# Kernel tuning notes

Hardware: AMD Instinct MI355X
Metric: run time of the kernel (lower is better)

The kernel has to match this reference:

```python
import jax, jax.numpy as jnp
import numpy as np

NUM_HEADS = 12
HEAD_DIM = 64  # d_out // num_heads = 768 // 12


def setup_inputs() -> dict:
    key = jax.random.key(0)
    k1, k2 = jax.random.split(key)
    x = jax.random.normal(k1, (2, 2048, 768), dtype=jnp.float32)
    # torch Linear weight: [d_out, d_in], y = x @ W.T
    Wq = jax.random.normal(k2, (768, 768), dtype=jnp.float32) * 0.02
    return {"x": x, "Wq": Wq}


def reference(x, Wq):
    b, n, d_in = x.shape
    H, hd = NUM_HEADS, HEAD_DIM
    d_out = H * hd
    # NOTE: the original module uses Wq for queries, keys AND values.
    qkv = x @ Wq.T                                   # [b, n, d_out]
    h = qkv.reshape(b, n, H, hd).transpose(0, 2, 1, 3)  # [b, H, n, hd]
    scores = jnp.einsum('bhqd,bhkd->bhqk', h, h)      # [b, H, n, n]
    causal = jnp.triu(jnp.ones((n, n), dtype=bool), k=1)
    scores = jnp.where(causal, -jnp.inf, scores)
    attn = jax.nn.softmax(scores / jnp.sqrt(jnp.float32(hd)), axis=-1)
    ctx = jnp.einsum('bhqk,bhkd->bhqd', attn, h)      # [b, H, n, hd]
    # faithful to source: transpose(-2,-1) -> [b, H, hd, n], then view(b, n, d_out)
    ctx = ctx.transpose(0, 1, 3, 2)
    return ctx.reshape(b, n, d_out)
```

## Files before the change

kernel.cpp:

```cpp
#include <hip/hip_runtime.h>
#include <math.h>

typedef __attribute__((ext_vector_type(8))) short  short8;
typedef __attribute__((ext_vector_type(4))) float  floatx4;

#define MFMA16(a, b, c) __builtin_amdgcn_mfma_f32_16x16x32_bf16(a, b, c, 0, 0, 0)

constexpr int NSEQ = 2048;
constexpr int DIN  = 768;
constexpr int NH   = 12;
constexpr float QSCALE = 0.18033688011112042f;

constexpr int PK = 72;

__device__ __forceinline__ ushort f2bf(float f) {
    unsigned u = __float_as_uint(f);
    u += 0x7FFF + ((u >> 16) & 1);
    return (ushort)(u >> 16);
}
__device__ __forceinline__ float bf2f(ushort u) {
    return __uint_as_float(((unsigned)u) << 16);
}
__device__ __forceinline__ unsigned cvt_pk_bf16(float lo, float hi) {
    unsigned r;
    asm("v_cvt_pk_bf16_f32 %0, %1, %2" : "=v"(r) : "v"(lo), "v"(hi));
    return r;
}
__device__ __forceinline__ short8 pk8(float4 a, float4 b) {
    union { unsigned u[4]; short8 s; } r;
    r.u[0] = cvt_pk_bf16(a.x, a.y);
    r.u[1] = cvt_pk_bf16(a.z, a.w);
    r.u[2] = cvt_pk_bf16(b.x, b.y);
    r.u[3] = cvt_pk_bf16(b.z, b.w);
    return r.s;
}
__device__ __forceinline__ void bar_lds() {
    asm volatile("s_waitcnt lgkmcnt(0)" ::: "memory");
    __builtin_amdgcn_s_barrier();
}

__global__ __launch_bounds__(256, 3)
void qkv_mfma(const float* __restrict__ x, const float* __restrict__ Wq,
              ushort* __restrict__ h)
{
    __shared__ ushort As[2][64 * PK];
    __shared__ ushort Bs[2][64 * PK];

    const int tid  = threadIdx.x;
    const int w    = tid >> 6;
    const int lane = tid & 63;
    const int m    = lane & 15;
    const int quad = lane >> 4;
    const int r0   = blockIdx.x * 64;
    const int c0   = blockIdx.y * 64;
    const int mrow0 = (w & 1) * 32;
    const int ncol0 = (w >> 1) * 32;

    const int srow = tid >> 3;
    const int scol = (tid & 7) * 8;

    floatx4 C[2][2] = {};
    float4 arf[2][2], brf[2][2];

    #pragma unroll
    for (int i = 0; i < 2; ++i) {
        const float* ax = x  + (size_t)(r0 + srow + i * 32) * DIN + scol;
        const float* bx = Wq + (size_t)(c0 + srow + i * 32) * DIN + scol;
        arf[i][0] = ((const float4*)ax)[0]; arf[i][1] = ((const float4*)ax)[1];
        brf[i][0] = ((const float4*)bx)[0]; brf[i][1] = ((const float4*)bx)[1];
    }
    #pragma unroll
    for (int i = 0; i < 2; ++i) {
        *(short8*)&As[0][(srow + i * 32) * PK + scol] = pk8(arf[i][0], arf[i][1]);
        *(short8*)&Bs[0][(srow + i * 32) * PK + scol] = pk8(brf[i][0], brf[i][1]);
    }
    #pragma unroll
    for (int i = 0; i < 2; ++i) {
        const float* ax = x  + (size_t)(r0 + srow + i * 32) * DIN + 64 + scol;
        const float* bx = Wq + (size_t)(c0 + srow + i * 32) * DIN + 64 + scol;
        arf[i][0] = ((const float4*)ax)[0]; arf[i][1] = ((const float4*)ax)[1];
        brf[i][0] = ((const float4*)bx)[0]; brf[i][1] = ((const float4*)bx)[1];
    }
    bar_lds();

    for (int kk = 0; kk < 12; ++kk) {
        const int cur = kk & 1;

        #pragma unroll
        for (int kt2 = 0; kt2 < 2; ++kt2) {
            short8 a0 = *(const short8*)&As[cur][(mrow0 + m)      * PK + kt2 * 32 + quad * 8];
            short8 a1 = *(const short8*)&As[cur][(mrow0 + 16 + m) * PK + kt2 * 32 + quad * 8];
            short8 b0 = *(const short8*)&Bs[cur][(ncol0 + m)      * PK + kt2 * 32 + quad * 8];
            short8 b1 = *(const short8*)&Bs[cur][(ncol0 + 16 + m) * PK + kt2 * 32 + quad * 8];
            C[0][0] = MFMA16(a0, b0, C[0][0]);
            C[0][1] = MFMA16(a0, b1, C[0][1]);
            C[1][0] = MFMA16(a1, b0, C[1][0]);
            C[1][1] = MFMA16(a1, b1, C[1][1]);
        }

        if (kk + 1 < 12) {
            const int nxt = cur ^ 1;
            #pragma unroll
            for (int i = 0; i < 2; ++i) {
                *(short8*)&As[nxt][(srow + i * 32) * PK + scol] = pk8(arf[i][0], arf[i][1]);
                *(short8*)&Bs[nxt][(srow + i * 32) * PK + scol] = pk8(brf[i][0], brf[i][1]);
            }
            if (kk + 2 < 12) {
                const int k0 = (kk + 2) * 64;
                #pragma unroll
                for (int i = 0; i < 2; ++i) {
                    const float* ax = x  + (size_t)(r0 + srow + i * 32) * DIN + k0 + scol;
                    const float* bx = Wq + (size_t)(c0 + srow + i * 32) * DIN + k0 + scol;
                    arf[i][0] = ((const float4*)ax)[0]; arf[i][1] = ((const float4*)ax)[1];
                    brf[i][0] = ((const float4*)bx)[0]; brf[i][1] = ((const float4*)bx)[1];
                }
            }
            bar_lds();
        }
    }

    #pragma unroll
    for (int mt = 0; mt < 2; ++mt)
        #pragma unroll
        for (int nt = 0; nt < 2; ++nt) {
            int cg = c0 + ncol0 + nt * 16 + m;
            int head = cg >> 6, d = cg & 63;
            #pragma unroll
            for (int r = 0; r < 4; ++r) {
                int rg = r0 + mrow0 + mt * 16 + quad * 4 + r;
                int b = rg >> 11, q = rg & 2047;
                h[((size_t)(b * NH + head) * NSEQ + q) * 64 + d] = f2bf(C[mt][nt][r]);
            }
        }
}

__global__ __launch_bounds__(256, 6)
void attn_mfma(const ushort* __restrict__ h, float* __restrict__ out)
{
    __shared__ ushort Ks[64 * PK];
    __shared__ ushort Vt[64 * PK];
    __shared__ ushort Ps[2 * 16 * PK];

    const int tid  = threadIdx.x;
    const int w    = tid >> 6;
    const int lane = tid & 63;
    const int m    = lane & 15;
    const int quad = lane >> 4;
    const int qsub = w & 1;
    const int khalf= w >> 1;

    const int xi = blockIdx.x;
    const int bh = blockIdx.y;
    const int qt = ((bh >> 2) & 1) ? xi : (63 - xi);
    const int q0 = qt * 32;
    const int wq = q0 + qsub * 16;
    const int nkt = (qt >> 1) + 1;
    const ushort* __restrict__ Hh = h + (size_t)bh * NSEQ * 64;
    ushort* Psw = Ps + qsub * 16 * PK;

    const int kr2  = (tid & 31) * 2;
    const int part = tid >> 5;
    const int db   = part * 8;

    short8 qa[2];
    #pragma unroll
    for (int kt2 = 0; kt2 < 2; ++kt2) {
        short8 raw = *(const short8*)(Hh + (size_t)(wq + m) * 64 + kt2 * 32 + quad * 8);
        #pragma unroll
        for (int j = 0; j < 8; ++j)
            qa[kt2][j] = (short)f2bf(bf2f((ushort)raw[j]) * QSCALE);
    }

    floatx4 O[4] = {};
    float lacc = 0.0f;

    short8 pre0, pre1;
    {
        const ushort* src = Hh + (size_t)kr2 * 64 + db;
        pre0 = *(const short8*)src;
        pre1 = *(const short8*)(src + 64);
    }

    for (int kt = 0; kt < nkt; ++kt) {
        bar_lds();

        *(short8*)&Ks[kr2       * PK + db] = pre0;
        *(short8*)&Ks[(kr2 + 1) * PK + db] = pre1;
        union { short8 v; ushort u[8]; } ua, ub;
        ua.v = pre0; ub.v = pre1;
        #pragma unroll
        for (int i = 0; i < 8; ++i)
            *(unsigned*)&Vt[(db + i) * PK + kr2] =
                (unsigned)ua.u[i] | ((unsigned)ub.u[i] << 16);
        if (kt + 1 < nkt) {
            const ushort* src = Hh + (size_t)((kt + 1) * 64 + kr2) * 64 + db;
            pre0 = *(const short8*)src;
            pre1 = *(const short8*)(src + 64);
        }
        bar_lds();

        floatx4 S[2] = {};
        #pragma unroll
        for (int kt2 = 0; kt2 < 2; ++kt2)
            #pragma unroll
            for (int mt2 = 0; mt2 < 2; ++mt2) {
                short8 ka = *(const short8*)
                    &Ks[(khalf * 32 + mt2 * 16 + m) * PK + kt2 * 32 + quad * 8];
                S[mt2] = MFMA16(ka, qa[kt2], S[mt2]);
            }

        const int lim  = wq + m - kt * 64;
        const bool diag = (kt == nkt - 1);
        #pragma unroll
        for (int mt2 = 0; mt2 < 2; ++mt2) {
            const int kb = (khalf * 2 + mt2) * 16 + quad * 4;
            float p0, p1, p2, p3;
            if (diag) {
                p0 = (kb + 0 <= lim) ? exp2f(S[mt2][0]) : 0.0f;
                p1 = (kb + 1 <= lim) ? exp2f(S[mt2][1]) : 0.0f;
                p2 = (kb + 2 <= lim) ? exp2f(S[mt2][2]) : 0.0f;
                p3 = (kb + 3 <= lim) ? exp2f(S[mt2][3]) : 0.0f;
            } else {
                p0 = exp2f(S[mt2][0]);
                p1 = exp2f(S[mt2][1]);
                p2 = exp2f(S[mt2][2]);
                p3 = exp2f(S[mt2][3]);
            }
            lacc += (p0 + p1) + (p2 + p3);
            uint2 pw;
            pw.x = cvt_pk_bf16(p0, p1);
            pw.y = cvt_pk_bf16(p2, p3);
            *(uint2*)&Psw[m * PK + kb] = pw;
        }

        short8 pb = *(const short8*)&Psw[m * PK + khalf * 32 + quad * 8];
        #pragma unroll
        for (int mt = 0; mt < 4; ++mt) {
            short8 va = *(const short8*)
                &Vt[(mt * 16 + m) * PK + khalf * 32 + quad * 8];
            O[mt] = MFMA16(va, pb, O[mt]);
        }
    }

    lacc += __shfl_xor(lacc, 16);
    lacc += __shfl_xor(lacc, 32);

    float* Om = (float*)&Ks[0];
    float* Lm = Om + 2 * 64 * 17;
    bar_lds();
    if (khalf == 1) {
        #pragma unroll
        for (int mt = 0; mt < 4; ++mt)
            #pragma unroll
            for (int r = 0; r < 4; ++r) {
                int d = mt * 16 + quad * 4 + r;
                Om[(qsub * 64 + d) * 17 + m] = O[mt][r];
            }
        if (quad == 0) Lm[qsub * 16 + m] = lacc;
    }
    bar_lds();
    if (khalf == 0) {
        float linv = 1.0f / (lacc + Lm[qsub * 16 + m]);
        #pragma unroll
        for (int mt = 0; mt < 4; ++mt)
            #pragma unroll
            for (int r = 0; r < 4; ++r) {
                int d = mt * 16 + quad * 4 + r;
                float v = O[mt][r] + Om[(qsub * 64 + d) * 17 + m];
                out[((size_t)bh * 64 + d) * NSEQ + q0 + qsub * 16 + m] = v * linv;
            }
    }
}

extern "C" void kernel_launch(void* const* d_in, const int* in_sizes, int n_in,
                              void* d_out, int out_size, void* d_ws, size_t ws_size,
                              hipStream_t stream)
{
    (void)in_sizes; (void)n_in; (void)out_size; (void)ws_size;
    const float* x  = (const float*)d_in[0];
    const float* Wq = (const float*)d_in[1];
    float* out = (float*)d_out;

    ushort* hb = (ushort*)d_ws;

    qkv_mfma<<<dim3(64, 12), dim3(256), 0, stream>>>(x, Wq, hb);
    attn_mfma<<<dim3(64, 24), dim3(256), 0, stream>>>(hb, out);
}
```

Before: 116.9 us.

## Rewrite attention with 32x32 MFMA, two waves, register-resident P via permlane swap

The attention kernel moves from four waves using 16x16x32 MFMA tiles to two waves using 32x32x16 MFMA tiles over the same 32-query block. Each wave now handles 32 keys and all 32 queries. The P matrix is kept in registers and rearranged with v_permlane32_swap instead of going through a shared-memory Ps buffer. K tiles in LDS get an XOR-style swizzle to cut bank conflicts. The aim is fewer LDS round trips and higher MFMA efficiency per instruction, at the cost of fewer threads per block, which may lower latency hiding and occupancy.

```diff
diff --git a/kernel.cpp b/kernel.cpp
--- a/kernel.cpp
+++ b/kernel.cpp
@@ -1,10 +1,12 @@
 #include <hip/hip_runtime.h>
 #include <math.h>
 
-typedef __attribute__((ext_vector_type(8))) short  short8;
-typedef __attribute__((ext_vector_type(4))) float  floatx4;
+typedef __attribute__((ext_vector_type(8)))  short short8;
+typedef __attribute__((ext_vector_type(4)))  float floatx4;
+typedef __attribute__((ext_vector_type(16))) float floatx16;
 
 #define MFMA16(a, b, c) __builtin_amdgcn_mfma_f32_16x16x32_bf16(a, b, c, 0, 0, 0)
+#define MFMA32(a, b, c) __builtin_amdgcn_mfma_f32_32x32x16_bf16(a, b, c, 0, 0, 0)
 
 constexpr int NSEQ = 2048;
 constexpr int DIN  = 768;
@@ -134,141 +136,149 @@
         }
 }
 
-__global__ __launch_bounds__(256, 6)
+__global__ __launch_bounds__(128, 3)
 void attn_mfma(const ushort* __restrict__ h, float* __restrict__ out)
 {
     __shared__ ushort Ks[64 * PK];
     __shared__ ushort Vt[64 * PK];
-    __shared__ ushort Ps[2 * 16 * PK];
 
     const int tid  = threadIdx.x;
     const int w    = tid >> 6;
     const int lane = tid & 63;
-    const int m    = lane & 15;
-    const int quad = lane >> 4;
-    const int qsub = w & 1;
-    const int khalf= w >> 1;
+    const int col  = lane & 31;
+    const int hi   = lane >> 5;
 
     const int xi = blockIdx.x;
     const int bh = blockIdx.y;
     const int qt = ((bh >> 2) & 1) ? xi : (63 - xi);
     const int q0 = qt * 32;
-    const int wq = q0 + qsub * 16;
     const int nkt = (qt >> 1) + 1;
     const ushort* __restrict__ Hh = h + (size_t)bh * NSEQ * 64;
-    ushort* Psw = Ps + qsub * 16 * PK;
-
-    const int kr2  = (tid & 31) * 2;
-    const int part = tid >> 5;
-    const int db   = part * 8;
-
-    short8 qa[2];
-    #pragma unroll
-    for (int kt2 = 0; kt2 < 2; ++kt2) {
-        short8 raw = *(const short8*)(Hh + (size_t)(wq + m) * 64 + kt2 * 32 + quad * 8);
+
+    const int kp = (tid & 15) * 4;
+    const int cc = tid >> 4;
+
+    short8 qa[4];
+    #pragma unroll
+    for (int s = 0; s < 4; ++s) {
+        short8 raw = *(const short8*)(Hh + (size_t)(q0 + col) * 64 + s * 16 + hi * 8);
         #pragma unroll
         for (int j = 0; j < 8; ++j)
-            qa[kt2][j] = (short)f2bf(bf2f((ushort)raw[j]) * QSCALE);
-    }
-
-    floatx4 O[4] = {};
+            qa[s][j] = (short)f2bf(bf2f((ushort)raw[j]) * QSCALE);
+    }
+
+    floatx16 O[2] = {};
     float lacc = 0.0f;
 
-    short8 pre0, pre1;
-    {
-        const ushort* src = Hh + (size_t)kr2 * 64 + db;
-        pre0 = *(const short8*)src;
-        pre1 = *(const short8*)(src + 64);
-    }
+    short8 fr[4];
+#define PREFETCH(KT) do {                                                      \
+    const ushort* s_ = Hh + ((size_t)(KT) * 64 + kp) * 64 + cc * 8;            \
+    fr[0] = *(const short8*)s_;                                                \
+    fr[1] = *(const short8*)(s_ + 64);                                         \
+    fr[2] = *(const short8*)(s_ + 128);                                        \
+    fr[3] = *(const short8*)(s_ + 192);                                        \
+} while (0)
+
+    PREFETCH(0);
 
     for (int kt = 0; kt < nkt; ++kt) {
         bar_lds();
 
-        *(short8*)&Ks[kr2       * PK + db] = pre0;
-        *(short8*)&Ks[(kr2 + 1) * PK + db] = pre1;
-        union { short8 v; ushort u[8]; } ua, ub;
-        ua.v = pre0; ub.v = pre1;
-        #pragma unroll
-        for (int i = 0; i < 8; ++i)
-            *(unsigned*)&Vt[(db + i) * PK + kr2] =
-                (unsigned)ua.u[i] | ((unsigned)ub.u[i] << 16);
-        if (kt + 1 < nkt) {
-            const ushort* src = Hh + (size_t)((kt + 1) * 64 + kr2) * 64 + db;
-            pre0 = *(const short8*)src;
-            pre1 = *(const short8*)(src + 64);
-        }
+        #pragma unroll
+        for (int j = 0; j < 4; ++j) {
+            int ky = kp + j;
+            *(short8*)&Ks[ky * PK + (((cc + 2 * (ky & 7)) & 7) << 3)] = fr[j];
+        }
+        {
+            union { short8 v; ushort u[8]; } f0, f1, f2, f3;
+            f0.v = fr[0]; f1.v = fr[1]; f2.v = fr[2]; f3.v = fr[3];
+            #pragma unroll
+            for (int i = 0; i < 8; ++i) {
+                uint2 dw;
+                dw.x = (unsigned)f0.u[i] | ((unsigned)f1.u[i] << 16);
+                dw.y = (unsigned)f2.u[i] | ((unsigned)f3.u[i] << 16);
+                *(uint2*)&Vt[(cc * 8 + i) * PK + kp] = dw;
+            }
+        }
+        if (kt + 1 < nkt) PREFETCH(kt + 1);
         bar_lds();
 
-        floatx4 S[2] = {};
-        #pragma unroll
-        for (int kt2 = 0; kt2 < 2; ++kt2)
-            #pragma unroll
-            for (int mt2 = 0; mt2 < 2; ++mt2) {
-                short8 ka = *(const short8*)
-                    &Ks[(khalf * 32 + mt2 * 16 + m) * PK + kt2 * 32 + quad * 8];
-                S[mt2] = MFMA16(ka, qa[kt2], S[mt2]);
-            }
-
-        const int lim  = wq + m - kt * 64;
+        floatx16 S = {};
+        #pragma unroll
+        for (int s = 0; s < 4; ++s) {
+            int key = w * 32 + col;
+            short8 ka = *(const short8*)
+                &Ks[key * PK + (((s * 2 + hi + 2 * (col & 7)) & 7) << 3)];
+            S = MFMA32(ka, qa[s], S);
+        }
+
         const bool diag = (kt == nkt - 1);
-        #pragma unroll
-        for (int mt2 = 0; mt2 < 2; ++mt2) {
-            const int kb = (khalf * 2 + mt2) * 16 + quad * 4;
-            float p0, p1, p2, p3;
-            if (diag) {
-                p0 = (kb + 0 <= lim) ? exp2f(S[mt2][0]) : 0.0f;
-                p1 = (kb + 1 <= lim) ? exp2f(S[mt2][1]) : 0.0f;
-                p2 = (kb + 2 <= lim) ? exp2f(S[mt2][2]) : 0.0f;
-                p3 = (kb + 3 <= lim) ? exp2f(S[mt2][3]) : 0.0f;
-            } else {
-                p0 = exp2f(S[mt2][0]);
-                p1 = exp2f(S[mt2][1]);
-                p2 = exp2f(S[mt2][2]);
-                p3 = exp2f(S[mt2][3]);
-            }
-            lacc += (p0 + p1) + (p2 + p3);
-            uint2 pw;
-            pw.x = cvt_pk_bf16(p0, p1);
-            pw.y = cvt_pk_bf16(p2, p3);
-            *(uint2*)&Psw[m * PK + kb] = pw;
-        }
-
-        short8 pb = *(const short8*)&Psw[m * PK + khalf * 32 + quad * 8];
-        #pragma unroll
-        for (int mt = 0; mt < 4; ++mt) {
-            short8 va = *(const short8*)
-                &Vt[(mt * 16 + m) * PK + khalf * 32 + quad * 8];
-            O[mt] = MFMA16(va, pb, O[mt]);
-        }
-    }
-
-    lacc += __shfl_xor(lacc, 16);
+        const int kbase = kt * 64 + w * 32;
+        const int qabs  = q0 + col;
+        unsigned bfr[2][4];
+        #pragma unroll
+        for (int h2 = 0; h2 < 2; ++h2) {
+            float p[8];
+            #pragma unroll
+            for (int j = 0; j < 8; ++j) {
+                const int reg = h2 * 8 + j;
+                const int kl  = (reg & 3) + 8 * (reg >> 2) + 4 * hi;
+                float pv = exp2f(S[reg]);
+                if (diag && (kbase + kl > qabs)) pv = 0.0f;
+                p[j] = pv;
+                lacc += pv;
+            }
+            unsigned a0 = cvt_pk_bf16(p[0], p[1]);
+            unsigned a1 = cvt_pk_bf16(p[2], p[3]);
+            unsigned a2 = cvt_pk_bf16(p[4], p[5]);
+            unsigned a3 = cvt_pk_bf16(p[6], p[7]);
+            asm volatile("v_permlane32_swap_b32 %0, %1" : "+v"(a0), "+v"(a2));
+            asm volatile("v_permlane32_swap_b32 %0, %1" : "+v"(a1), "+v"(a3));
+            bfr[h2][0] = a0; bfr[h2][1] = a1; bfr[h2][2] = a2; bfr[h2][3] = a3;
+        }
+
+        #pragma unroll
+        for (int h2 = 0; h2 < 2; ++h2) {
+            union { unsigned u[4]; short8 v; } pb;
+            pb.u[0] = bfr[h2][0]; pb.u[1] = bfr[h2][1];
+            pb.u[2] = bfr[h2][2]; pb.u[3] = bfr[h2][3];
+            #pragma unroll
+            for (int dt = 0; dt < 2; ++dt) {
+                short8 va = *(const short8*)
+                    &Vt[(dt * 32 + col) * PK + w * 32 + h2 * 16 + hi * 8];
+                O[dt] = MFMA32(va, pb.v, O[dt]);
+            }
+        }
+    }
+#undef PREFETCH
+
     lacc += __shfl_xor(lacc, 32);
 
-    float* Om = (float*)&Ks[0];
-    float* Lm = Om + 2 * 64 * 17;
+    float* OmA = (float*)&Ks[0];
+    float* OmB = OmA + 32 * 33;
+    float* Lg  = OmB + 32 * 33;
+
     bar_lds();
-    if (khalf == 1) {
-        #pragma unroll
-        for (int mt = 0; mt < 4; ++mt)
-            #pragma unroll
-            for (int r = 0; r < 4; ++r) {
-                int d = mt * 16 + quad * 4 + r;
-                Om[(qsub * 64 + d) * 17 + m] = O[mt][r];
-            }
-        if (quad == 0) Lm[qsub * 16 + m] = lacc;
+    {
+        float* Om = (w == 0) ? OmA : OmB;
+        #pragma unroll
+        for (int reg = 0; reg < 16; ++reg) {
+            const int dl = (reg & 3) + 8 * (reg >> 2) + 4 * hi;
+            Om[dl * 33 + col] = (w == 0) ? O[1][reg] : O[0][reg];
+        }
+        if (hi == 0) Lg[w * 32 + col] = lacc;
     }
     bar_lds();
-    if (khalf == 0) {
-        float linv = 1.0f / (lacc + Lm[qsub * 16 + m]);
-        #pragma unroll
-        for (int mt = 0; mt < 4; ++mt)
-            #pragma unroll
-            for (int r = 0; r < 4; ++r) {
-                int d = mt * 16 + quad * 4 + r;
-                float v = O[mt][r] + Om[(qsub * 64 + d) * 17 + m];
-                out[((size_t)bh * 64 + d) * NSEQ + q0 + qsub * 16 + m] = v * linv;
-            }
+    {
+        const float linv = 1.0f / (Lg[col] + Lg[32 + col]);
+        float* Om = (w == 0) ? OmB : OmA;
+        #pragma unroll
+        for (int reg = 0; reg < 16; ++reg) {
+            const int dl = (reg & 3) + 8 * (reg >> 2) + 4 * hi;
+            const int d  = w * 32 + dl;
+            const float v = ((w == 0) ? O[0][reg] : O[1][reg]) + Om[dl * 33 + col];
+            out[((size_t)bh * 64 + d) * NSEQ + q0 + col] = v * linv;
+        }
     }
 }
 
@@ -284,5 +294,5 @@
     ushort* hb = (ushort*)d_ws;
 
     qkv_mfma<<<dim3(64, 12), dim3(256), 0, stream>>>(x, Wq, hb);
-    attn_mfma<<<dim3(64, 24), dim3(256), 0, stream>>>(hb, out);
-}
+    attn_mfma<<<dim3(64, 24), dim3(128), 0, stream>>>(hb, out);
+}
```

Result: slower. 119.6 us (+2.4%).
